# Kernel tuning notes

Measured on AMD Instinct MI355X. Metric: run time of the kernel, lower is better.

Reference implementation:

```python
import jax, jax.numpy as jnp
import numpy as np

B, C_IN, T = 32, 192, 8192
H, N_PH, OUT = 192, 1024, 4
EPS = 1e-5


def setup_inputs() -> dict:
    key = jax.random.key(0)
    ks = jax.random.split(key, 12)
    s = 0.02
    return {
        "x": jax.random.normal(ks[0], (B, C_IN, T), jnp.float32),
        "x_mask": jnp.ones((B, 1, N_PH), jnp.float32),
        "w": jax.random.randint(ks[1], (B, 1, N_PH), 0, 8, jnp.int32),
        "pre_w": jax.random.normal(ks[2], (H, C_IN), jnp.float32) * s,
        "pre_b": jnp.zeros((H,), jnp.float32),
        "conv0_w": jax.random.normal(ks[3], (H, H, 3), jnp.float32) * s,
        "conv0_b": jnp.zeros((H,), jnp.float32),
        "ln0_g": jnp.ones((H,), jnp.float32),
        "ln0_b": jnp.zeros((H,), jnp.float32),
        "conv1_w": jax.random.normal(ks[4], (H, H, 3), jnp.float32) * s,
        "conv1_b": jnp.zeros((H,), jnp.float32),
        "ln1_g": jnp.ones((H,), jnp.float32),
        "ln1_b": jnp.zeros((H,), jnp.float32),
        "lin_w": jax.random.normal(ks[5], (OUT, H), jnp.float32) * s,
        "lin_b": jnp.zeros((OUT,), jnp.float32),
    }


def _segment_mean(x, w2):
    # x: [B, C, T] frames; w2: [B, n_ph] int durations.
    # Faithful to the torch double loop: phoneme j pools frames
    # [cumsum(w)[j-1] : cumsum(w)[j]); w==0 -> zeros.
    ends = jnp.cumsum(w2, axis=1)                      # [B, n_ph]
    t = jnp.arange(x.shape[2], dtype=ends.dtype)       # [T]
    ph_id = jax.vmap(lambda e: jnp.searchsorted(e, t, side="right"))(ends)  # [B, T]
    # segment sums over frames; extra segment n_ph catches out-of-range frames
    sums = jax.vmap(lambda xt, ids: jax.ops.segment_sum(xt, ids, num_segments=N_PH + 1))(
        x.transpose(0, 2, 1), ph_id
    )                                                  # [B, n_ph+1, C]
    sums = sums[:, :N_PH].transpose(0, 2, 1)           # [B, C, n_ph]
    denom = jnp.maximum(w2, 1).astype(x.dtype)[:, None, :]
    return jnp.where(w2[:, None, :] > 0, sums / denom, 0.0)


def _conv3(x, k, b):
    y = jax.lax.conv_general_dilated(x, k, (1,), [(1, 1)],
                                     dimension_numbers=("NCH", "OIH", "NCH"))
    return y + b[None, :, None]


def _ln(x, g, b):
    # channel-dim LayerNorm for [B, C, T] (VITS modules.LayerNorm)
    m = jnp.mean(x, axis=1, keepdims=True)
    v = jnp.mean(jnp.square(x - m), axis=1, keepdims=True)
    return (x - m) * jax.lax.rsqrt(v + EPS) * g[None, :, None] + b[None, :, None]


def reference(x, x_mask, w, pre_w, pre_b, conv0_w, conv0_b, ln0_g, ln0_b,
              conv1_w, conv1_b, ln1_g, ln1_b, lin_w, lin_b):
    w2 = w.reshape(w.shape[0], -1).astype(jnp.int32)
    spec = _segment_mean(x, w2)                                 # [B, C_in, n_ph]
    h = jnp.einsum("bct,hc->bht", spec, pre_w) + pre_b[None, :, None]
    # block 0: conv -> relu -> LN (dropout is identity at eval), mask before each layer
    h = _conv3(h * x_mask, conv0_w, conv0_b)
    h = jax.nn.relu(h * x_mask)
    h = _ln(h * x_mask, ln0_g, ln0_b)
    h = h * x_mask  # dropout(p=0.1) at eval = identity; mask still applied
    # block 1
    h = _conv3(h * x_mask, conv1_w, conv1_b)
    h = jax.nn.relu(h * x_mask)
    h = _ln(h * x_mask, ln1_g, ln1_b)
    h = h * x_mask
    p = jnp.einsum("bht,oh->bot", h, lin_w) + lin_b[None, :, None]
    return p * x_mask
```

## Files before the change

kernel.cpp:

```cpp
#include <hip/hip_runtime.h>
#include <hip/hip_bf16.h>

#define B 32
#define C_IN 192
#define T 8192
#define H 192
#define N_PH 1024
#define OUT 4
#define ROW_MAX 7168
#define PROWS (N_PH + 2)
#define ROWP (2 * H)

typedef __attribute__((ext_vector_type(8))) short short8;
typedef __attribute__((ext_vector_type(4))) float f32x4;
typedef unsigned short ushort_t;

__device__ inline ushort_t f2bf(float f) {
    unsigned u = __builtin_bit_cast(unsigned, f);
    unsigned r = u + 0x7fffu + ((u >> 16) & 1u);
    return (ushort_t)(r >> 16);
}
__device__ inline float bf2f(ushort_t h) {
    unsigned u = ((unsigned)h) << 16;
    return __builtin_bit_cast(float, u);
}
__device__ inline void split_bf(float x, ushort_t& hi, ushort_t& lo) {
    hi = f2bf(x);
    lo = f2bf(x - bf2f(hi));
}

__global__ __launch_bounds__(1024) void scan_kernel(const int* __restrict__ w,
                                                    int* __restrict__ ends) {
    int b = blockIdx.x;
    __shared__ int s[N_PH];
    int tid = threadIdx.x;
    s[tid] = w[b * N_PH + tid];
    __syncthreads();
    for (int off = 1; off < N_PH; off <<= 1) {
        int v = (tid >= off) ? s[tid - off] : 0;
        __syncthreads();
        s[tid] += v;
        __syncthreads();
    }
    ends[b * N_PH + tid] = s[tid];
}

__global__ __launch_bounds__(256) void segmean_kernel(const float* __restrict__ x,
                                                      const int* __restrict__ ends,
                                                      float* __restrict__ spec) {
    int bc = blockIdx.x;
    int b = bc / C_IN;
    int c = bc % C_IN;
    __shared__ int e_s[N_PH];
    __shared__ float row[ROW_MAX];
    int tid = threadIdx.x;
    for (int j = tid; j < N_PH; j += 256) e_s[j] = ends[b * N_PH + j];
    __syncthreads();
    int emax = e_s[N_PH - 1];
    if (emax > ROW_MAX) emax = ROW_MAX;
    const float4* xr4 = (const float4*)(x + ((size_t)b * C_IN + c) * T);
    float4* row4 = (float4*)row;
    int nv = (emax + 3) >> 2;
    for (int t = tid; t < nv; t += 256) row4[t] = xr4[t];
    __syncthreads();
    float* sp = spec + ((size_t)b * C_IN + c) * N_PH;
    for (int j = tid; j < N_PH; j += 256) {
        int s0 = j ? e_s[j - 1] : 0;
        int e0 = e_s[j];
        float sum = 0.f;
        for (int t = s0; t < e0; ++t) sum += row[t];
        sp[j] = (e0 > s0) ? sum / (float)(e0 - s0) : 0.f;
    }
}

__global__ __launch_bounds__(256) void transpose_spec_kernel(const float* __restrict__ spec,
                                                             ushort_t* __restrict__ specT) {
    int jt = blockIdx.x * 32;
    int ct = (blockIdx.y % (C_IN / 32)) * 32;
    int b  = blockIdx.y / (C_IN / 32);
    __shared__ float tile[32][33];
    int tx = threadIdx.x & 31;
    int ty = threadIdx.x >> 5;
    const float* sb = spec + ((size_t)b * C_IN + ct) * N_PH + jt;
    for (int r = ty; r < 32; r += 8) tile[r][tx] = sb[(size_t)r * N_PH + tx];
    __syncthreads();
    ushort_t* ob = specT + ((size_t)b * N_PH + jt) * ROWP + ct;
    for (int r = ty; r < 32; r += 8) {
        ushort_t hi, lo;
        split_bf(tile[tx][r], hi, lo);
        ob[(size_t)r * ROWP + tx] = hi;
        ob[(size_t)r * ROWP + H + tx] = lo;
    }
}

__global__ void wfrag_cvt_kernel(const float* __restrict__ w, ushort_t* __restrict__ wtf,
                                 int taps) {
    int idx = blockIdx.x * 256 + threadIdx.x;
    int ntot = taps * 6 * 12 * 512;
    if (idx >= ntot) return;
    int j  = idx & 7;
    int l  = (idx >> 3) & 63;
    int slot = idx >> 9;
    int nt = slot % 12;
    int ss = (slot / 12) % 6;
    int kt = slot / 72;
    int o  = nt * 16 + (l & 15);
    int i  = ss * 32 + ((l >> 4) << 3) + j;
    float v = (taps == 1) ? w[o * C_IN + i]
                          : w[(o * H + i) * 3 + kt];
    ushort_t hi, lo;
    split_bf(v, hi, lo);
    wtf[idx] = hi;
    wtf[idx + ntot] = lo;
}

__global__ __launch_bounds__(256) void gemm_fused_kernel(
    const ushort_t* __restrict__ in, int in_rows,
    const ushort_t* __restrict__ wt,
    const float* __restrict__ bias,
    const float* __restrict__ mask,
    const float* __restrict__ g, const float* __restrict__ beta,
    ushort_t* __restrict__ out,
    int taps, int do_ln, int nmask)
{
    int b  = blockIdx.y;
    int t0 = blockIdx.x * 64;
    int tid = threadIdx.x;
    int lane = tid & 63;
    int wv = tid >> 6;
    int mhalf = wv & 1;
    int nhalf = wv >> 1;

    __shared__ float ep[64][193];
    __shared__ float g_s[H], b_s[H], m_s[64], mstat[64], rstat[64];
    if (tid < H) { g_s[tid] = do_ln ? g[tid] : 1.f; b_s[tid] = do_ln ? beta[tid] : 0.f; }
    if (tid < 64) m_s[tid] = mask[b * N_PH + t0 + tid];

    short8 z8 = {0, 0, 0, 0, 0, 0, 0, 0};
    if (t0 == 0 && tid < ROWP / 8)
        *(short8*)(out + (size_t)b * PROWS * ROWP + tid * 8) = z8;
    if (t0 == N_PH - 64 && tid < ROWP / 8)
        *(short8*)(out + ((size_t)b * PROWS + N_PH + 1) * ROWP + tid * 8) = z8;

    int m  = lane & 15;
    int kg = (lane >> 4) << 3;
    int ntotw = taps * 36864;
    int pad = taps >> 1;

    const ushort_t* inb = in + (size_t)b * in_rows * ROWP;
    int trow = t0 + mhalf * 32 + m;

    f32x4 acc[2][6];
#pragma unroll
    for (int ntl = 0; ntl < 6; ++ntl) {
        float bb = bias[(nhalf * 6 + ntl) * 16 + m];
        acc[0][ntl] = (f32x4){bb, bb, bb, bb};
        acc[1][ntl] = (f32x4){bb, bb, bb, bb};
    }

#pragma unroll 1
    for (int kt = 0; kt < taps; ++kt) {
        const ushort_t* arow = inb + (long)(trow + kt - pad) * ROWP;
#pragma unroll 1
        for (int s = 0; s < 6; ++s) {
            int ko = s * 32 + kg;
            short8 ah0 = *(const short8*)(arow + ko);
            short8 al0 = *(const short8*)(arow + H + ko);
            short8 ah1 = *(const short8*)(arow + 16 * ROWP + ko);
            short8 al1 = *(const short8*)(arow + 16 * ROWP + H + ko);
            const ushort_t* wbase = wt + ((size_t)((kt * 6 + s) * 12 + nhalf * 6) << 9)
                                  + (lane << 3);
#pragma unroll
            for (int ntl = 0; ntl < 6; ++ntl) {
                short8 bh8 = *(const short8*)(wbase + (ntl << 9));
                short8 bl8 = *(const short8*)(wbase + (ntl << 9) + ntotw);
                acc[0][ntl] = __builtin_amdgcn_mfma_f32_16x16x32_bf16(ah0, bh8, acc[0][ntl], 0, 0, 0);
                acc[0][ntl] = __builtin_amdgcn_mfma_f32_16x16x32_bf16(al0, bh8, acc[0][ntl], 0, 0, 0);
                acc[0][ntl] = __builtin_amdgcn_mfma_f32_16x16x32_bf16(ah0, bl8, acc[0][ntl], 0, 0, 0);
                acc[1][ntl] = __builtin_amdgcn_mfma_f32_16x16x32_bf16(ah1, bh8, acc[1][ntl], 0, 0, 0);
                acc[1][ntl] = __builtin_amdgcn_mfma_f32_16x16x32_bf16(al1, bh8, acc[1][ntl], 0, 0, 0);
                acc[1][ntl] = __builtin_amdgcn_mfma_f32_16x16x32_bf16(ah1, bl8, acc[1][ntl], 0, 0, 0);
            }
        }
    }

    __syncthreads();

    int rbase = (lane >> 4) << 2;
#pragma unroll
    for (int mh = 0; mh < 2; ++mh) {
#pragma unroll
        for (int ntl = 0; ntl < 6; ++ntl) {
            int o = (nhalf * 6 + ntl) * 16 + m;
#pragma unroll
            for (int r = 0; r < 4; ++r) {
                int t_loc = mhalf * 32 + mh * 16 + rbase + r;
                float mm = m_s[t_loc];
                float v = acc[mh][ntl][r];
                if (do_ln) {
                    v = fmaxf(v * mm, 0.f) * mm;
                } else {
                    for (int q = 0; q < nmask; ++q) v *= mm;
                }
                ep[t_loc][o] = v;
            }
        }
    }
    __syncthreads();

    if (do_ln && tid < 64) {
        float s = 0.f, ss = 0.f;
        for (int c = 0; c < H; ++c) {
            float v = ep[tid][c];
            s += v;
            ss += v * v;
        }
        float mean = s * (1.f / (float)H);
        mstat[tid] = mean;
        rstat[tid] = rsqrtf(ss * (1.f / (float)H) - mean * mean + 1e-5f);
    }
    __syncthreads();

    int row = tid >> 2;
    int q = tid & 3;
    float mean = 0.f, rstd = 1.f, mfac = 1.f;
    if (do_ln) {
        mean = mstat[row];
        rstd = rstat[row];
        float mk = m_s[row];
        mfac = (nmask == 2) ? mk * mk : mk;
    }
    ushort_t* orow = out + ((size_t)b * PROWS + t0 + row + 1) * ROWP + q * 48;
#pragma unroll
    for (int i0 = 0; i0 < 48; i0 += 8) {
        ushort_t th[8], tl[8];
#pragma unroll
        for (int k2 = 0; k2 < 8; ++k2) {
            int c = q * 48 + i0 + k2;
            float v = ep[row][c];
            float y = do_ln ? ((v - mean) * rstd * g_s[c] + b_s[c]) * mfac : v;
            split_bf(y, th[k2], tl[k2]);
        }
        *(short8*)(orow + i0) = *(short8*)th;
        *(short8*)(orow + H + i0) = *(short8*)tl;
    }
}

__global__ __launch_bounds__(256) void final_kernel(const ushort_t* __restrict__ in,
                                                    const float* __restrict__ lw,
                                                    const float* __restrict__ lb,
                                                    const float* __restrict__ mask,
                                                    float* __restrict__ out) {
    int b = blockIdx.y;
    int t0 = blockIdx.x * 64;
    __shared__ ushort_t s_in[64 * ROWP];
    __shared__ float w_s[OUT][H];
    int tid = threadIdx.x;
    for (int i = tid; i < OUT * H; i += 256) w_s[i / H][i % H] = lw[i];
    const short8* g8 = (const short8*)(in + ((size_t)b * PROWS + t0 + 1) * ROWP);
    short8* s8 = (short8*)s_in;
    for (int i = tid; i < 64 * ROWP / 8; i += 256) s8[i] = g8[i];
    __syncthreads();
    int row = tid >> 2;
    int q = tid & 3;
    const ushort_t* rp = s_in + row * ROWP + q * 48;
    float a0 = 0.f, a1 = 0.f, a2 = 0.f, a3 = 0.f;
#pragma unroll
    for (int i0 = 0; i0 < 48; i0 += 8) {
        short8 vh = *(const short8*)(rp + i0);
        short8 vl = *(const short8*)(rp + H + i0);
#pragma unroll
        for (int k = 0; k < 8; ++k) {
            int c = q * 48 + i0 + k;
            float v = bf2f((ushort_t)vh[k]) + bf2f((ushort_t)vl[k]);
            a0 += w_s[0][c] * v;
            a1 += w_s[1][c] * v;
            a2 += w_s[2][c] * v;
            a3 += w_s[3][c] * v;
        }
    }
    a0 += __shfl_xor(a0, 1); a0 += __shfl_xor(a0, 2);
    a1 += __shfl_xor(a1, 1); a1 += __shfl_xor(a1, 2);
    a2 += __shfl_xor(a2, 1); a2 += __shfl_xor(a2, 2);
    a3 += __shfl_xor(a3, 1); a3 += __shfl_xor(a3, 2);
    if (q == 0) {
        int t = t0 + row;
        float m = mask[b * N_PH + t];
        float* ob = out + (size_t)b * OUT * N_PH + t;
        ob[0 * N_PH] = (a0 + lb[0]) * m;
        ob[1 * N_PH] = (a1 + lb[1]) * m;
        ob[2 * N_PH] = (a2 + lb[2]) * m;
        ob[3 * N_PH] = (a3 + lb[3]) * m;
    }
}

extern "C" void kernel_launch(void* const* d_in, const int* in_sizes, int n_in,
                              void* d_out, int out_size, void* d_ws, size_t ws_size,
                              hipStream_t stream) {
    const float* x      = (const float*)d_in[0];
    const float* x_mask = (const float*)d_in[1];
    const int*   w      = (const int*)d_in[2];
    const float* pre_w  = (const float*)d_in[3];
    const float* pre_b  = (const float*)d_in[4];
    const float* conv0_w = (const float*)d_in[5];
    const float* conv0_b = (const float*)d_in[6];
    const float* ln0_g   = (const float*)d_in[7];
    const float* ln0_b   = (const float*)d_in[8];
    const float* conv1_w = (const float*)d_in[9];
    const float* conv1_b = (const float*)d_in[10];
    const float* ln1_g   = (const float*)d_in[11];
    const float* ln1_b   = (const float*)d_in[12];
    const float* lin_w   = (const float*)d_in[13];
    const float* lin_b   = (const float*)d_in[14];
    float* out = (float*)d_out;

    char* ws = (char*)d_ws;
    size_t off = 0;
    int* ends = (int*)(ws + off);           off += (size_t)B * N_PH * sizeof(int);
    float* spec = (float*)(ws + off);       off += (size_t)B * C_IN * N_PH * sizeof(float);
    ushort_t* bufA = (ushort_t*)(ws + off); off += (size_t)B * PROWS * ROWP * sizeof(ushort_t);
    ushort_t* bufB = (ushort_t*)(ws + off); off += (size_t)B * PROWS * ROWP * sizeof(ushort_t);
    ushort_t* wpre = (ushort_t*)(ws + off); off += (size_t)2 * 36864 * sizeof(ushort_t);
    ushort_t* w0t  = (ushort_t*)(ws + off); off += (size_t)2 * 110592 * sizeof(ushort_t);
    ushort_t* w1t  = (ushort_t*)(ws + off); off += (size_t)2 * 110592 * sizeof(ushort_t);
    ushort_t* specT = bufB;

    scan_kernel<<<B, 1024, 0, stream>>>(w, ends);
    wfrag_cvt_kernel<<<(36864 + 255) / 256, 256, 0, stream>>>(pre_w, wpre, 1);
    wfrag_cvt_kernel<<<(110592 + 255) / 256, 256, 0, stream>>>(conv0_w, w0t, 3);
    wfrag_cvt_kernel<<<(110592 + 255) / 256, 256, 0, stream>>>(conv1_w, w1t, 3);

    segmean_kernel<<<B * C_IN, 256, 0, stream>>>(x, ends, spec);
    dim3 gt(N_PH / 32, (C_IN / 32) * B);
    transpose_spec_kernel<<<gt, 256, 0, stream>>>(spec, specT);

    dim3 gg(N_PH / 64, B);
    gemm_fused_kernel<<<gg, 256, 0, stream>>>(specT, N_PH, wpre, pre_b, x_mask,
                                              ln0_g, ln0_b, bufA, 1, 0, 1);
    gemm_fused_kernel<<<gg, 256, 0, stream>>>(bufA + ROWP, PROWS, w0t, conv0_b, x_mask,
                                              ln0_g, ln0_b, bufB, 3, 1, 2);
    gemm_fused_kernel<<<gg, 256, 0, stream>>>(bufB + ROWP, PROWS, w1t, conv1_b, x_mask,
                                              ln1_g, ln1_b, bufA, 3, 1, 1);

    dim3 gf(N_PH / 64, B);
    final_kernel<<<gf, 256, 0, stream>>>(bufA, lin_w, lin_b, x_mask, out);
}
```

Measured before the change: 419.9 us.

## Fuse scan into segmean, merge weight converts, fuse final linear, double-buffer GEMM loads

Moves the duration prefix-sum into each segmean block, which removes the separate scan kernel and its ends buffer. The three weight-conversion launches become one kernel. The final 4-output linear is folded into the last conv GEMM epilogue, reading LN output from LDS instead of a bf16 hi/lo buffer. The GEMM K loop now software-prefetches the next iteration's operands into registers, which raises register pressure. The ROW_MAX clamp is also dropped, which is only safe when durations never exceed the row buffer.

```diff
diff --git a/kernel.cpp b/kernel.cpp
--- a/kernel.cpp
+++ b/kernel.cpp
@@ -29,35 +29,33 @@
     lo = f2bf(x - bf2f(hi));
 }
 
-__global__ __launch_bounds__(1024) void scan_kernel(const int* __restrict__ w,
-                                                    int* __restrict__ ends) {
-    int b = blockIdx.x;
-    __shared__ int s[N_PH];
-    int tid = threadIdx.x;
-    s[tid] = w[b * N_PH + tid];
-    __syncthreads();
-    for (int off = 1; off < N_PH; off <<= 1) {
-        int v = (tid >= off) ? s[tid - off] : 0;
-        __syncthreads();
-        s[tid] += v;
-        __syncthreads();
-    }
-    ends[b * N_PH + tid] = s[tid];
-}
-
 __global__ __launch_bounds__(256) void segmean_kernel(const float* __restrict__ x,
-                                                      const int* __restrict__ ends,
+                                                      const int* __restrict__ wdur,
                                                       float* __restrict__ spec) {
     int bc = blockIdx.x;
     int b = bc / C_IN;
     int c = bc % C_IN;
     __shared__ int e_s[N_PH];
+    __shared__ int part[256];
     __shared__ float row[ROW_MAX];
     int tid = threadIdx.x;
-    for (int j = tid; j < N_PH; j += 256) e_s[j] = ends[b * N_PH + j];
+    int4 w4 = ((const int4*)(wdur + b * N_PH))[tid];
+    int c0 = w4.x, c1 = c0 + w4.y, c2 = c1 + w4.z, c3 = c2 + w4.w;
+    part[tid] = c3;
+    __syncthreads();
+    for (int off = 1; off < 256; off <<= 1) {
+        int v = (tid >= off) ? part[tid - off] : 0;
+        __syncthreads();
+        part[tid] += v;
+        __syncthreads();
+    }
+    int pre = tid ? part[tid - 1] : 0;
+    e_s[4 * tid + 0] = pre + c0;
+    e_s[4 * tid + 1] = pre + c1;
+    e_s[4 * tid + 2] = pre + c2;
+    e_s[4 * tid + 3] = pre + c3;
     __syncthreads();
     int emax = e_s[N_PH - 1];
-    if (emax > ROW_MAX) emax = ROW_MAX;
     const float4* xr4 = (const float4*)(x + ((size_t)b * C_IN + c) * T);
     float4* row4 = (float4*)row;
     int nv = (emax + 3) >> 2;
@@ -93,11 +91,8 @@
     }
 }
 
-__global__ void wfrag_cvt_kernel(const float* __restrict__ w, ushort_t* __restrict__ wtf,
-                                 int taps) {
-    int idx = blockIdx.x * 256 + threadIdx.x;
-    int ntot = taps * 6 * 12 * 512;
-    if (idx >= ntot) return;
+__device__ inline void wfrag_one(const float* __restrict__ w, ushort_t* __restrict__ wtf,
+                                 int taps, int idx, int ntot) {
     int j  = idx & 7;
     int l  = (idx >> 3) & 63;
     int slot = idx >> 9;
@@ -106,13 +101,48 @@
     int kt = slot / 72;
     int o  = nt * 16 + (l & 15);
     int i  = ss * 32 + ((l >> 4) << 3) + j;
-    float v = (taps == 1) ? w[o * C_IN + i]
-                          : w[(o * H + i) * 3 + kt];
+    float v = (taps == 1) ? w[o * C_IN + i] : w[(o * H + i) * 3 + kt];
     ushort_t hi, lo;
     split_bf(v, hi, lo);
     wtf[idx] = hi;
     wtf[idx + ntot] = lo;
 }
+__global__ void wfrag_all_kernel(const float* __restrict__ pw, const float* __restrict__ w0,
+                                 const float* __restrict__ w1,
+                                 ushort_t* __restrict__ wpre, ushort_t* __restrict__ w0t,
+                                 ushort_t* __restrict__ w1t) {
+    int idx = blockIdx.x * 256 + threadIdx.x;
+    const int n1 = 36864, n3 = 110592;
+    if (idx < n1) { wfrag_one(pw, wpre, 1, idx, n1); return; }
+    idx -= n1;
+    if (idx < n3) { wfrag_one(w0, w0t, 3, idx, n3); return; }
+    idx -= n3;
+    if (idx < n3) wfrag_one(w1, w1t, 3, idx, n3);
+}
+
+#define LOADOPS(IT, AH0, AL0, AH1, AL1, BH, BL) do {                              \
+    int kt_ = (IT) / 6, s_ = (IT) - kt_ * 6;                                      \
+    const ushort_t* arow_ = inb + (long)(trow + kt_ - pad) * ROWP + s_ * 32 + kg; \
+    AH0 = *(const short8*)(arow_);                                                \
+    AL0 = *(const short8*)(arow_ + H);                                            \
+    AH1 = *(const short8*)(arow_ + 16 * ROWP);                                    \
+    AL1 = *(const short8*)(arow_ + 16 * ROWP + H);                                \
+    const ushort_t* wb_ = wt + ((size_t)((kt_ * 6 + s_) * 12 + nhalf * 6) << 9)   \
+                        + (lane << 3);                                            \
+    _Pragma("unroll") for (int n_ = 0; n_ < 6; ++n_) {                            \
+        BH[n_] = *(const short8*)(wb_ + (n_ << 9));                               \
+        BL[n_] = *(const short8*)(wb_ + (n_ << 9) + ntotw); }                     \
+} while (0)
+
+#define DOMFMA(AH0, AL0, AH1, AL1, BH, BL) do {                                             \
+    _Pragma("unroll") for (int n_ = 0; n_ < 6; ++n_) {                                      \
+        acc[0][n_] = __builtin_amdgcn_mfma_f32_16x16x32_bf16(AH0, BH[n_], acc[0][n_], 0,0,0); \
+        acc[0][n_] = __builtin_amdgcn_mfma_f32_16x16x32_bf16(AL0, BH[n_], acc[0][n_], 0,0,0); \
+        acc[0][n_] = __builtin_amdgcn_mfma_f32_16x16x32_bf16(AH0, BL[n_], acc[0][n_], 0,0,0); \
+        acc[1][n_] = __builtin_amdgcn_mfma_f32_16x16x32_bf16(AH1, BH[n_], acc[1][n_], 0,0,0); \
+        acc[1][n_] = __builtin_amdgcn_mfma_f32_16x16x32_bf16(AL1, BH[n_], acc[1][n_], 0,0,0); \
+        acc[1][n_] = __builtin_amdgcn_mfma_f32_16x16x32_bf16(AH1, BL[n_], acc[1][n_], 0,0,0); } \
+} while (0)
 
 __global__ __launch_bounds__(256) void gemm_fused_kernel(
     const ushort_t* __restrict__ in, int in_rows,
@@ -121,7 +151,9 @@
     const float* __restrict__ mask,
     const float* __restrict__ g, const float* __restrict__ beta,
     ushort_t* __restrict__ out,
-    int taps, int do_ln, int nmask)
+    const float* __restrict__ lw, const float* __restrict__ lb,
+    float* __restrict__ fout,
+    int taps, int do_ln, int nmask, int fin)
 {
     int b  = blockIdx.y;
     int t0 = blockIdx.x * 64;
@@ -137,10 +169,12 @@
     if (tid < 64) m_s[tid] = mask[b * N_PH + t0 + tid];
 
     short8 z8 = {0, 0, 0, 0, 0, 0, 0, 0};
-    if (t0 == 0 && tid < ROWP / 8)
-        *(short8*)(out + (size_t)b * PROWS * ROWP + tid * 8) = z8;
-    if (t0 == N_PH - 64 && tid < ROWP / 8)
-        *(short8*)(out + ((size_t)b * PROWS + N_PH + 1) * ROWP + tid * 8) = z8;
+    if (!fin) {
+        if (t0 == 0 && tid < ROWP / 8)
+            *(short8*)(out + (size_t)b * PROWS * ROWP + tid * 8) = z8;
+        if (t0 == N_PH - 64 && tid < ROWP / 8)
+            *(short8*)(out + ((size_t)b * PROWS + N_PH + 1) * ROWP + tid * 8) = z8;
+    }
 
     int m  = lane & 15;
     int kg = (lane >> 4) << 3;
@@ -158,30 +192,16 @@
         acc[1][ntl] = (f32x4){bb, bb, bb, bb};
     }
 
+    short8 pah0, pal0, pah1, pal1, pbh[6], pbl[6];
+    short8 qah0, qal0, qah1, qal1, qbh[6], qbl[6];
+    int iters = taps * 6;
+    LOADOPS(0, pah0, pal0, pah1, pal1, pbh, pbl);
 #pragma unroll 1
-    for (int kt = 0; kt < taps; ++kt) {
-        const ushort_t* arow = inb + (long)(trow + kt - pad) * ROWP;
-#pragma unroll 1
-        for (int s = 0; s < 6; ++s) {
-            int ko = s * 32 + kg;
-            short8 ah0 = *(const short8*)(arow + ko);
-            short8 al0 = *(const short8*)(arow + H + ko);
-            short8 ah1 = *(const short8*)(arow + 16 * ROWP + ko);
-            short8 al1 = *(const short8*)(arow + 16 * ROWP + H + ko);
-            const ushort_t* wbase = wt + ((size_t)((kt * 6 + s) * 12 + nhalf * 6) << 9)
-                                  + (lane << 3);
-#pragma unroll
-            for (int ntl = 0; ntl < 6; ++ntl) {
-                short8 bh8 = *(const short8*)(wbase + (ntl << 9));
-                short8 bl8 = *(const short8*)(wbase + (ntl << 9) + ntotw);
-                acc[0][ntl] = __builtin_amdgcn_mfma_f32_16x16x32_bf16(ah0, bh8, acc[0][ntl], 0, 0, 0);
-                acc[0][ntl] = __builtin_amdgcn_mfma_f32_16x16x32_bf16(al0, bh8, acc[0][ntl], 0, 0, 0);
-                acc[0][ntl] = __builtin_amdgcn_mfma_f32_16x16x32_bf16(ah0, bl8, acc[0][ntl], 0, 0, 0);
-                acc[1][ntl] = __builtin_amdgcn_mfma_f32_16x16x32_bf16(ah1, bh8, acc[1][ntl], 0, 0, 0);
-                acc[1][ntl] = __builtin_amdgcn_mfma_f32_16x16x32_bf16(al1, bh8, acc[1][ntl], 0, 0, 0);
-                acc[1][ntl] = __builtin_amdgcn_mfma_f32_16x16x32_bf16(ah1, bl8, acc[1][ntl], 0, 0, 0);
-            }
-        }
+    for (int it = 0; it < iters; it += 2) {
+        LOADOPS(it + 1, qah0, qal0, qah1, qal1, qbh, qbl);
+        DOMFMA(pah0, pal0, pah1, pal1, pbh, pbl);
+        if (it + 2 < iters) LOADOPS(it + 2, pah0, pal0, pah1, pal1, pbh, pbl);
+        DOMFMA(qah0, qal0, qah1, qal1, qbh, qbl);
     }
 
     __syncthreads();
@@ -223,6 +243,32 @@
 
     int row = tid >> 2;
     int q = tid & 3;
+    if (fin) {
+        float mean = mstat[row], rstd = rstat[row], mk = m_s[row];
+        float a0 = 0.f, a1 = 0.f, a2 = 0.f, a3 = 0.f;
+#pragma unroll 1
+        for (int c = q * 48; c < q * 48 + 48; ++c) {
+            float y = ((ep[row][c] - mean) * rstd * g_s[c] + b_s[c]) * mk;
+            a0 += lw[0 * H + c] * y;
+            a1 += lw[1 * H + c] * y;
+            a2 += lw[2 * H + c] * y;
+            a3 += lw[3 * H + c] * y;
+        }
+        a0 += __shfl_xor(a0, 1); a0 += __shfl_xor(a0, 2);
+        a1 += __shfl_xor(a1, 1); a1 += __shfl_xor(a1, 2);
+        a2 += __shfl_xor(a2, 1); a2 += __shfl_xor(a2, 2);
+        a3 += __shfl_xor(a3, 1); a3 += __shfl_xor(a3, 2);
+        if (q == 0) {
+            int t = t0 + row;
+            float* ob = fout + (size_t)b * OUT * N_PH + t;
+            ob[0 * N_PH] = (a0 + lb[0]) * mk;
+            ob[1 * N_PH] = (a1 + lb[1]) * mk;
+            ob[2 * N_PH] = (a2 + lb[2]) * mk;
+            ob[3 * N_PH] = (a3 + lb[3]) * mk;
+        }
+        return;
+    }
+
     float mean = 0.f, rstd = 1.f, mfac = 1.f;
     if (do_ln) {
         mean = mstat[row];
@@ -243,54 +289,6 @@
         }
         *(short8*)(orow + i0) = *(short8*)th;
         *(short8*)(orow + H + i0) = *(short8*)tl;
-    }
-}
-
-__global__ __launch_bounds__(256) void final_kernel(const ushort_t* __restrict__ in,
-                                                    const float* __restrict__ lw,
-                                                    const float* __restrict__ lb,
-                                                    const float* __restrict__ mask,
-                                                    float* __restrict__ out) {
-    int b = blockIdx.y;
-    int t0 = blockIdx.x * 64;
-    __shared__ ushort_t s_in[64 * ROWP];
-    __shared__ float w_s[OUT][H];
-    int tid = threadIdx.x;
-    for (int i = tid; i < OUT * H; i += 256) w_s[i / H][i % H] = lw[i];
-    const short8* g8 = (const short8*)(in + ((size_t)b * PROWS + t0 + 1) * ROWP);
-    short8* s8 = (short8*)s_in;
-    for (int i = tid; i < 64 * ROWP / 8; i += 256) s8[i] = g8[i];
-    __syncthreads();
-    int row = tid >> 2;
-    int q = tid & 3;
-    const ushort_t* rp = s_in + row * ROWP + q * 48;
-    float a0 = 0.f, a1 = 0.f, a2 = 0.f, a3 = 0.f;
-#pragma unroll
-    for (int i0 = 0; i0 < 48; i0 += 8) {
-        short8 vh = *(const short8*)(rp + i0);
-        short8 vl = *(const short8*)(rp + H + i0);
-#pragma unroll
-        for (int k = 0; k < 8; ++k) {
-            int c = q * 48 + i0 + k;
-            float v = bf2f((ushort_t)vh[k]) + bf2f((ushort_t)vl[k]);
-            a0 += w_s[0][c] * v;
-            a1 += w_s[1][c] * v;
-            a2 += w_s[2][c] * v;
-            a3 += w_s[3][c] * v;
-        }
-    }
-    a0 += __shfl_xor(a0, 1); a0 += __shfl_xor(a0, 2);
-    a1 += __shfl_xor(a1, 1); a1 += __shfl_xor(a1, 2);
-    a2 += __shfl_xor(a2, 1); a2 += __shfl_xor(a2, 2);
-    a3 += __shfl_xor(a3, 1); a3 += __shfl_xor(a3, 2);
-    if (q == 0) {
-        int t = t0 + row;
-        float m = mask[b * N_PH + t];
-        float* ob = out + (size_t)b * OUT * N_PH + t;
-        ob[0 * N_PH] = (a0 + lb[0]) * m;
-        ob[1 * N_PH] = (a1 + lb[1]) * m;
-        ob[2 * N_PH] = (a2 + lb[2]) * m;
-        ob[3 * N_PH] = (a3 + lb[3]) * m;
     }
 }
 
@@ -316,7 +314,6 @@
 
     char* ws = (char*)d_ws;
     size_t off = 0;
-    int* ends = (int*)(ws + off);           off += (size_t)B * N_PH * sizeof(int);
     float* spec = (float*)(ws + off);       off += (size_t)B * C_IN * N_PH * sizeof(float);
     ushort_t* bufA = (ushort_t*)(ws + off); off += (size_t)B * PROWS * ROWP * sizeof(ushort_t);
     ushort_t* bufB = (ushort_t*)(ws + off); off += (size_t)B * PROWS * ROWP * sizeof(ushort_t);
@@ -325,23 +322,21 @@
     ushort_t* w1t  = (ushort_t*)(ws + off); off += (size_t)2 * 110592 * sizeof(ushort_t);
     ushort_t* specT = bufB;
 
-    scan_kernel<<<B, 1024, 0, stream>>>(w, ends);
-    wfrag_cvt_kernel<<<(36864 + 255) / 256, 256, 0, stream>>>(pre_w, wpre, 1);
-    wfrag_cvt_kernel<<<(110592 + 255) / 256, 256, 0, stream>>>(conv0_w, w0t, 3);
-    wfrag_cvt_kernel<<<(110592 + 255) / 256, 256, 0, stream>>>(conv1_w, w1t, 3);
-
-    segmean_kernel<<<B * C_IN, 256, 0, stream>>>(x, ends, spec);
+    wfrag_all_kernel<<<(36864 + 2 * 110592 + 255) / 256, 256, 0, stream>>>(
+        pre_w, conv0_w, conv1_w, wpre, w0t, w1t);
+
+    segmean_kernel<<<B * C_IN, 256, 0, stream>>>(x, w, spec);
     dim3 gt(N_PH / 32, (C_IN / 32) * B);
     transpose_spec_kernel<<<gt, 256, 0, stream>>>(spec, specT);
 
     dim3 gg(N_PH / 64, B);
     gemm_fused_kernel<<<gg, 256, 0, stream>>>(specT, N_PH, wpre, pre_b, x_mask,
-                                              ln0_g, ln0_b, bufA, 1, 0, 1);
+                                              ln0_g, ln0_b, bufA,
+                                              nullptr, nullptr, nullptr, 1, 0, 1, 0);
     gemm_fused_kernel<<<gg, 256, 0, stream>>>(bufA + ROWP, PROWS, w0t, conv0_b, x_mask,
-                                              ln0_g, ln0_b, bufB, 3, 1, 2);
+                                              ln0_g, ln0_b, bufB,
+                                              nullptr, nullptr, nullptr, 3, 1, 2, 0);
     gemm_fused_kernel<<<gg, 256, 0, stream>>>(bufB + ROWP, PROWS, w1t, conv1_b, x_mask,
-                                              ln1_g, ln1_b, bufA, 3, 1, 1);
-
-    dim3 gf(N_PH / 64, B);
-    final_kernel<<<gf, 256, 0, stream>>>(bufA, lin_w, lin_b, x_mask, out);
-}
+                                              ln1_g, ln1_b, bufA,
+                                              lin_w, lin_b, out, 3, 1, 1, 1);
+}
```

Result: faster. 397.6 us (-5.3%).
